# Optimization experiments

Measured on AMD Instinct MI355X. Metric: run time of the kernel, lower is better.

Reference implementation:

```python
import jax, jax.numpy as jnp
import numpy as np

B, T, C = 2, 2048, 768
N_HEADS = 12
HEAD = C // N_HEADS


def setup_inputs() -> dict:
    key = jax.random.key(0)
    k1, k2, k3 = jax.random.split(key, 3)
    x = jax.random.normal(k1, (B, T, C), dtype=jnp.float32)
    # torch Linear weights: [out_features, in_features]
    W_attn = jax.random.normal(k2, (3 * C, C), dtype=jnp.float32) * 0.02
    W_proj = jax.random.normal(k3, (C, C), dtype=jnp.float32) * 0.02
    return {"x": x, "W_attn": W_attn, "W_proj": W_proj}


def reference(x, W_attn, W_proj):
    b, t, c = x.shape
    qkv = jnp.einsum('btc,oc->bto', x, W_attn)  # [B,T,3C]
    q, k, v = jnp.split(qkv, 3, axis=-1)
    # [B, H, T, D]
    q = q.reshape(b, t, N_HEADS, HEAD).transpose(0, 2, 1, 3)
    k = k.reshape(b, t, N_HEADS, HEAD).transpose(0, 2, 1, 3)
    v = v.reshape(b, t, N_HEADS, HEAD).transpose(0, 2, 1, 3)
    scale = 1.0 / jnp.sqrt(jnp.asarray(HEAD, dtype=x.dtype))
    wei = jnp.einsum('bhqd,bhkd->bhqk', q, k) * scale  # [B,H,T,T]
    causal = jnp.tril(jnp.ones((t, t), dtype=bool))
    wei = jnp.where(causal[None, None], wei, jnp.asarray(-jnp.inf, dtype=wei.dtype))
    wei = jax.nn.softmax(wei, axis=-1)  # dropout p=0 -> identity
    out = jnp.einsum('bhqk,bhkd->bhqd', wei, v)
    out = out.transpose(0, 2, 1, 3).reshape(b, t, c)
    out = jnp.einsum('btc,oc->bto', out, W_proj)
    return out
```

## Files before the change

kernel.cpp:

```cpp
#include <hip/hip_runtime.h>

#define T_DIM 2048
#define C_DIM 768
#define NH    12
#define HD    64
#define KDIM  768
#define JOBS_PER_XCD 96

typedef __attribute__((ext_vector_type(8))) short short8;
typedef __attribute__((ext_vector_type(4))) float f32x4;
typedef unsigned short u16;

__device__ __forceinline__ u16 f2bf(float f) {
    unsigned int u = __builtin_bit_cast(unsigned int, f);
    u = (u + 0x7fffu + ((u >> 16) & 1u)) >> 16;
    return (u16)u;
}
__device__ __forceinline__ f32x4 max4(f32x4 a, f32x4 b) {
    f32x4 r; r[0]=fmaxf(a[0],b[0]); r[1]=fmaxf(a[1],b[1]);
    r[2]=fmaxf(a[2],b[2]); r[3]=fmaxf(a[3],b[3]); return r;
}
__device__ __forceinline__ unsigned int cvtpk(float a, float b) {
    unsigned int r;
    asm("v_cvt_pk_bf16_f32 %0, %1, %2" : "=v"(r) : "v"(a), "v"(b));
    return r;
}
__device__ __forceinline__ void gload16(const u16* g, u16* l) {
    __builtin_amdgcn_global_load_lds(
        (const __attribute__((address_space(1))) unsigned int*)g,
        (__attribute__((address_space(3))) unsigned int*)l, 16, 0, 0);
}

#define NX  (4096 * 768)
#define NWA (2304 * 768)
#define NWP (768 * 768)
#define TOT4 ((NX + NWA + NWP) / 4)

__global__ __launch_bounds__(256) void convert_all(
    const float* __restrict__ x, const float* __restrict__ wa,
    const float* __restrict__ wp, u16* __restrict__ xb,
    u16* __restrict__ wab, u16* __restrict__ wpb, int* __restrict__ counters)
{
    if (blockIdx.x == 0 && threadIdx.x < 8) counters[threadIdx.x] = 0;
    for (int i4 = blockIdx.x * 256 + threadIdx.x; i4 < TOT4; i4 += gridDim.x * 256) {
        int i = i4 * 4;
        const float* src; u16* dst; int off;
        if (i < NX)            { src = x;  dst = xb;  off = i; }
        else if (i < NX + NWA) { src = wa; dst = wab; off = i - NX; }
        else                   { src = wp; dst = wpb; off = i - NX - NWA; }
        float4 v = *(const float4*)&src[off];
        ushort4 o;
        o.x = f2bf(v.x); o.y = f2bf(v.y); o.z = f2bf(v.z); o.w = f2bf(v.w);
        *(ushort4*)&dst[off] = o;
    }
}

__global__ __launch_bounds__(256) void gemm_qkv(
    const u16* __restrict__ A, const u16* __restrict__ Wt,
    u16* __restrict__ qb, u16* __restrict__ kb, u16* __restrict__ vtb)
{
    __shared__ __align__(16) u16 AsL[2][128][32];
    __shared__ __align__(16) u16 BsL[2][128][32];

    const int tid = threadIdx.x;
    const int orig = blockIdx.x;
    const int wg = (orig & 7) * 72 + (orig >> 3);
    const int bm = (wg / 18) * 128;
    const int bn = (wg % 18) * 128;

    const int w = tid >> 6, l = tid & 63;
    const int wr = (w >> 1) * 64, wc = (w & 1) * 64;
    const int lrow = l & 15, lg = l >> 4;
    const int lr4 = l >> 2, lc4 = l & 3;

    f32x4 acc[4][4];
    const f32x4 zero4 = {0.f, 0.f, 0.f, 0.f};
#pragma unroll
    for (int mi = 0; mi < 4; ++mi)
#pragma unroll
        for (int ni = 0; ni < 4; ++ni) acc[mi][ni] = zero4;

    auto STAGE = [&](int buf, int k0) {
#pragma unroll
        for (int i = 0; i < 2; ++i) {
            const int rb = w * 32 + i * 16;
            const int row = rb + lr4;
            const int sc = (lc4 ^ (row & 3)) * 8;
            gload16(&A [(size_t)(bm + row) * KDIM + k0 + sc], &AsL[buf][rb][0]);
            gload16(&Wt[(size_t)(bn + row) * KDIM + k0 + sc], &BsL[buf][rb][0]);
        }
    };

    int cur = 0;
    STAGE(0, 0);
    for (int k0 = 0; k0 < KDIM; k0 += 32) {
        __syncthreads();
        if (k0 + 32 < KDIM) STAGE(cur ^ 1, k0 + 32);

        short8 af[4], bf[4];
#pragma unroll
        for (int mi = 0; mi < 4; ++mi)
            af[mi] = *(const short8*)&AsL[cur][wr + mi * 16 + lrow][(lg ^ (lrow & 3)) * 8];
#pragma unroll
        for (int ni = 0; ni < 4; ++ni)
            bf[ni] = *(const short8*)&BsL[cur][wc + ni * 16 + lrow][(lg ^ (lrow & 3)) * 8];
#pragma unroll
        for (int mi = 0; mi < 4; ++mi)
#pragma unroll
            for (int ni = 0; ni < 4; ++ni)
                acc[mi][ni] = __builtin_amdgcn_mfma_f32_16x16x32_bf16(
                    af[mi], bf[ni], acc[mi][ni], 0, 0, 0);
        cur ^= 1;
    }

#pragma unroll
    for (int ni = 0; ni < 4; ++ni) {
        const int colbase = bn + wc + ni * 16;
        const int which = colbase / C_DIM;
        const int h = (colbase % C_DIM) / HD;
        const int d = (colbase % HD) + lrow;
        const float qs = (which == 0) ? 0.18033688011112042f : 1.0f;
#pragma unroll
        for (int mi = 0; mi < 4; ++mi) {
            const int t0 = bm + wr + mi * 16 + lg * 4;
            const int bb2 = t0 >> 11, tt = t0 & 2047;
            const size_t bhoff = (size_t)(bb2 * NH + h);
            if (which == 2) {
                ushort4 pv;
                pv.x = f2bf(acc[mi][ni][0]); pv.y = f2bf(acc[mi][ni][1]);
                pv.z = f2bf(acc[mi][ni][2]); pv.w = f2bf(acc[mi][ni][3]);
                *(ushort4*)&vtb[(bhoff * HD + d) * T_DIM + tt] = pv;
            } else {
                u16* dst = (which == 0) ? qb : kb;
#pragma unroll
                for (int jj = 0; jj < 4; ++jj)
                    dst[(bhoff * T_DIM + tt + jj) * HD + d] = f2bf(acc[mi][ni][jj] * qs);
            }
        }
    }
}

__global__ __launch_bounds__(256) void gemm_proj(
    const u16* __restrict__ A, const u16* __restrict__ Wt,
    float* __restrict__ dense)
{
    __shared__ __align__(16) u16 As[64][40];
    __shared__ __align__(16) u16 Bs[128][40];

    const int tid = threadIdx.x;
    const int orig = blockIdx.x;
    const int wg = (orig & 7) * 48 + (orig >> 3);
    const int bm = (wg / 6) * 64, bn = (wg % 6) * 128;

    const int w = tid >> 6, l = tid & 63;
    const int wr = (w >> 1) * 32, wc = (w & 1) * 64;
    const int lrow = l & 15, lg = l >> 4;

    const int srow = tid >> 2;
    const int scol = (tid & 3) * 8;

    f32x4 acc[2][4];
    const f32x4 zero4 = {0.f, 0.f, 0.f, 0.f};
#pragma unroll
    for (int mi = 0; mi < 2; ++mi)
#pragma unroll
        for (int ni = 0; ni < 4; ++ni) acc[mi][ni] = zero4;

    uint4 ra0 = *(const uint4*)&A [(size_t)(bm + srow)      * KDIM + scol];
    uint4 rb0 = *(const uint4*)&Wt[(size_t)(bn + srow)      * KDIM + scol];
    uint4 rb1 = *(const uint4*)&Wt[(size_t)(bn + 64 + srow) * KDIM + scol];

    for (int k0 = 0; k0 < KDIM; k0 += 32) {
        __syncthreads();
        *(uint4*)&As[srow][scol]      = ra0;
        *(uint4*)&Bs[srow][scol]      = rb0;
        *(uint4*)&Bs[64 + srow][scol] = rb1;
        __syncthreads();

        if (k0 + 32 < KDIM) {
            ra0 = *(const uint4*)&A [(size_t)(bm + srow)      * KDIM + k0 + 32 + scol];
            rb0 = *(const uint4*)&Wt[(size_t)(bn + srow)      * KDIM + k0 + 32 + scol];
            rb1 = *(const uint4*)&Wt[(size_t)(bn + 64 + srow) * KDIM + k0 + 32 + scol];
        }

        short8 af[2], bf[4];
#pragma unroll
        for (int mi = 0; mi < 2; ++mi)
            af[mi] = *(const short8*)&As[wr + mi * 16 + lrow][lg * 8];
#pragma unroll
        for (int ni = 0; ni < 4; ++ni)
            bf[ni] = *(const short8*)&Bs[wc + ni * 16 + lrow][lg * 8];
#pragma unroll
        for (int mi = 0; mi < 2; ++mi)
#pragma unroll
            for (int ni = 0; ni < 4; ++ni)
                acc[mi][ni] = __builtin_amdgcn_mfma_f32_16x16x32_bf16(
                    af[mi], bf[ni], acc[mi][ni], 0, 0, 0);
    }

#pragma unroll
    for (int ni = 0; ni < 4; ++ni) {
        const int col = bn + wc + ni * 16 + lrow;
#pragma unroll
        for (int mi = 0; mi < 2; ++mi) {
            const int m0 = bm + wr + mi * 16 + lg * 4;
#pragma unroll
            for (int jj = 0; jj < 4; ++jj)
                dense[(size_t)(m0 + jj) * C_DIM + col] = acc[mi][ni][jj];
        }
    }
}

__global__ __launch_bounds__(256, 2) void attn_mfma(
    const u16* __restrict__ q, const u16* __restrict__ k,
    const u16* __restrict__ vt, u16* __restrict__ aw, int* __restrict__ counters)
{
    __shared__ __align__(16) u16 KsL [2][128][64];
    __shared__ __align__(16) u16 VtsL[2][64][128];
    __shared__ __align__(16) u16 Ps  [4][16][72];
    __shared__ int job_s;

    const int tid = threadIdx.x, w = tid >> 6, l = tid & 63;
    const int lrow = l & 15, lg = l >> 4;
    const int lr8 = l >> 3, lc8 = l & 7;
    const int lr16 = l >> 4, lc16 = l & 15;
    const int xcdi = blockIdx.x & 7;
    const f32x4 zero4 = {0.f, 0.f, 0.f, 0.f};

    for (;;) {
        __syncthreads();
        if (tid == 0) job_s = atomicAdd(&counters[xcdi], 1);
        __syncthreads();
        const int j = job_s;
        if (j >= JOBS_PER_XCD) break;

        const int qt = 31 - (j / 3);
        const int bh = xcdi * 3 + (j - (j / 3) * 3);
        const int bb = bh / NH, hh = bh % NH;
        const int qbase = qt * 64 + w * 16;
        const int qg = qbase + lrow;

        const u16* Qp = q  + (size_t)bh * T_DIM * HD;
        const u16* Kp = k  + (size_t)bh * T_DIM * HD;
        const u16* Vp = vt + (size_t)bh * HD * T_DIM;

        const short8 aq0 = *(const short8*)&Qp[(size_t)(qbase + lrow) * HD + lg * 8];
        const short8 aq1 = *(const short8*)&Qp[(size_t)(qbase + lrow) * HD + 32 + lg * 8];

        f32x4 o0[4], o1[4];
#pragma unroll
        for (int n = 0; n < 4; ++n) { o0[n] = zero4; o1[n] = zero4; }
        float m0 = -3.0e38f, l0 = 0.0f;
        float m1 = -3.0e38f, l1 = 0.0f;

        auto STAGE = [&](int buf, int kk0) {
#pragma unroll
            for (int i = 0; i < 4; ++i) {
                const int rb = w * 32 + i * 8;
                const int row = rb + lr8;
                gload16(&Kp[(size_t)(kk0 + row) * HD + ((lc8 ^ (row & 7)) * 8)],
                        &KsL[buf][rb][0]);
            }
#pragma unroll
            for (int i = 0; i < 4; ++i) {
                const int db = w * 16 + i * 4;
                const int d = db + lr16;
                gload16(&Vp[(size_t)d * T_DIM + kk0 + ((lc16 ^ (d & 15)) * 8)],
                        &VtsL[buf][db][0]);
            }
        };

        auto PROCESS = [&](f32x4* s, int sub, int kk0, bool masked,
                           float& mr, float& lr_, f32x4* oo) {
            if (masked) {
#pragma unroll
                for (int n = 0; n < 4; ++n)
#pragma unroll
                    for (int jj = 0; jj < 4; ++jj)
                        if (kk0 + sub * 64 + n * 16 + lg * 4 + jj > qg)
                            s[n][jj] = -3.0e38f;
            }
            f32x4 t2 = max4(max4(s[0], s[1]), max4(s[2], s[3]));
            float rm = fmaxf(fmaxf(t2[0], t2[1]), fmaxf(t2[2], t2[3]));
            rm = fmaxf(rm, __shfl_xor(rm, 16));
            rm = fmaxf(rm, __shfl_xor(rm, 32));
            const float m_new = fmaxf(mr, rm);
            const float alpha = exp2f(mr - m_new);
            mr = m_new;
#pragma unroll
            for (int n = 0; n < 4; ++n)
#pragma unroll
                for (int jj = 0; jj < 4; ++jj)
                    s[n][jj] = exp2f(s[n][jj] - m_new);
            f32x4 a2 = (s[0] + s[1]) + (s[2] + s[3]);
            float rs = (a2[0] + a2[1]) + (a2[2] + a2[3]);
            rs += __shfl_xor(rs, 16);
            rs += __shfl_xor(rs, 32);
            lr_ = lr_ * alpha + rs;
#pragma unroll
            for (int n = 0; n < 4; ++n) {
                uint2 pr;
                pr.x = cvtpk(s[n][0], s[n][1]);
                pr.y = cvtpk(s[n][2], s[n][3]);
                *(uint2*)&Ps[w][lrow][n * 16 + lg * 4] = pr;
            }
#pragma unroll
            for (int jj = 0; jj < 4; ++jj) {
                const float aj = __shfl(alpha, lg * 4 + jj);
                oo[0][jj] *= aj; oo[1][jj] *= aj; oo[2][jj] *= aj; oo[3][jj] *= aj;
            }
            const short8 ap0 = *(const short8*)&Ps[w][lrow][lg * 8];
            const short8 ap1 = *(const short8*)&Ps[w][lrow][32 + lg * 8];
            const int cur = (kk0 >> 7) & 1;
#pragma unroll
            for (int n = 0; n < 4; ++n) {
                const int row = n * 16 + lrow;
                const short8 bv0 = *(const short8*)
                    &VtsL[cur][row][((sub * 8 + lg) ^ lrow) * 8];
                const short8 bv1 = *(const short8*)
                    &VtsL[cur][row][((sub * 8 + 4 + lg) ^ lrow) * 8];
                oo[n] = __builtin_amdgcn_mfma_f32_16x16x32_bf16(ap0, bv0, oo[n], 0, 0, 0);
                oo[n] = __builtin_amdgcn_mfma_f32_16x16x32_bf16(ap1, bv1, oo[n], 0, 0, 0);
            }
        };

        const int nkt = qt / 2 + 1;
        int cur = 0;
        STAGE(0, 0);
        for (int kt = 0; kt < nkt; ++kt) {
            const int kk0 = kt * 128;
            __syncthreads();
            if (kt + 1 < nkt) STAGE(cur ^ 1, kk0 + 128);

            const bool last = (kt == nkt - 1);
            const int nsub = (last && (qt & 1) == 0) ? 1 : 2;

            f32x4 s0[4], s1[4];
#pragma unroll
            for (int n = 0; n < 4; ++n) {
                const int row = n * 16 + lrow;
                const short8 kf0 = *(const short8*)&KsL[cur][row][((lg)     ^ (lrow & 7)) * 8];
                const short8 kf1 = *(const short8*)&KsL[cur][row][((lg + 4) ^ (lrow & 7)) * 8];
                s0[n] = __builtin_amdgcn_mfma_f32_16x16x32_bf16(kf0, aq0, zero4, 0, 0, 0);
                s0[n] = __builtin_amdgcn_mfma_f32_16x16x32_bf16(kf1, aq1, s0[n], 0, 0, 0);
            }
            if (nsub == 2) {
#pragma unroll
                for (int n = 0; n < 4; ++n) {
                    const int row = 64 + n * 16 + lrow;
                    const short8 kf0 = *(const short8*)&KsL[cur][row][((lg)     ^ (lrow & 7)) * 8];
                    const short8 kf1 = *(const short8*)&KsL[cur][row][((lg + 4) ^ (lrow & 7)) * 8];
                    s1[n] = __builtin_amdgcn_mfma_f32_16x16x32_bf16(kf0, aq0, zero4, 0, 0, 0);
                    s1[n] = __builtin_amdgcn_mfma_f32_16x16x32_bf16(kf1, aq1, s1[n], 0, 0, 0);
                }
            }

            PROCESS(s0, 0, kk0, last && nsub == 1, m0, l0, o0);
            if (nsub == 2) PROCESS(s1, 1, kk0, last, m1, l1, o1);

            cur ^= 1;
        }

        const float mf = fmaxf(m0, m1);
        const float a0 = exp2f(m0 - mf);
        const float a1 = exp2f(m1 - mf);
        const float inv = 1.0f / (l0 * a0 + l1 * a1);
#pragma unroll
        for (int jj = 0; jj < 4; ++jj) {
            const int qrow = lg * 4 + jj;
            const float a0j = __shfl(a0, qrow);
            const float a1j = __shfl(a1, qrow);
            const float invj = __shfl(inv, qrow);
            const size_t m = (size_t)bb * T_DIM + qbase + qrow;
#pragma unroll
            for (int n = 0; n < 4; ++n)
                aw[m * C_DIM + hh * HD + n * 16 + lrow] =
                    f2bf((o0[n][jj] * a0j + o1[n][jj] * a1j) * invj);
        }
    }
}

extern "C" void kernel_launch(void* const* d_in, const int* in_sizes, int n_in,
                              void* d_out, int out_size, void* d_ws, size_t ws_size,
                              hipStream_t stream) {
    const float* x      = (const float*)d_in[0];
    const float* W_attn = (const float*)d_in[1];
    const float* W_proj = (const float*)d_in[2];
    float* out = (float*)d_out;

    char* ws = (char*)d_ws;
    u16* xb  = (u16*)ws;                       ws += (size_t)NX * 2;
    u16* wab = (u16*)ws;                       ws += (size_t)NWA * 2;
    u16* wpb = (u16*)ws;                       ws += (size_t)NWP * 2;
    u16* qb  = (u16*)ws;                       ws += (size_t)24 * T_DIM * HD * 2;
    u16* kb  = (u16*)ws;                       ws += (size_t)24 * T_DIM * HD * 2;
    u16* vtb = (u16*)ws;                       ws += (size_t)24 * T_DIM * HD * 2;
    u16* awb = (u16*)ws;                       ws += (size_t)4096 * C_DIM * 2;
    int* cnt = (int*)ws;

    convert_all<<<2048, 256, 0, stream>>>(x, W_attn, W_proj, xb, wab, wpb, cnt);

    gemm_qkv<<<576, 256, 0, stream>>>(xb, wab, qb, kb, vtb);

    attn_mfma<<<512, 256, 0, stream>>>(qb, kb, vtb, awb, cnt);

    gemm_proj<<<384, 256, 0, stream>>>(awb, wpb, out);
}
```

Baseline: 99.17 us.

## Schedule attention per wave with direct global K/V fragment loads instead of LDS

The attention kernel now has each wave claim its own job: 32 query rows for one batch-head, split into two 16-row groups. Jobs come from a per-XCD atomic counter padded onto separate cache lines, replacing the block-wide atomic and its two barriers. K and V fragments are read straight from global memory into registers and shared by both query groups, so LDS double buffering and per-tile __syncthreads are gone. This removes block-level synchronisation and gives finer-grained load balance across the causal triangle, at the cost of losing the asynchronous prefetch and cross-wave K/V reuse through LDS, which leaves more load latency exposed.

```diff
diff --git a/kernel.cpp b/kernel.cpp
--- a/kernel.cpp
+++ b/kernel.cpp
@@ -5,7 +5,7 @@
 #define NH    12
 #define HD    64
 #define KDIM  768
-#define JOBS_PER_XCD 96
+#define JOBS_PER_XCD 192
 
 typedef __attribute__((ext_vector_type(8))) short short8;
 typedef __attribute__((ext_vector_type(4))) float f32x4;
@@ -41,7 +41,7 @@
     const float* __restrict__ wp, u16* __restrict__ xb,
     u16* __restrict__ wab, u16* __restrict__ wpb, int* __restrict__ counters)
 {
-    if (blockIdx.x == 0 && threadIdx.x < 8) counters[threadIdx.x] = 0;
+    if (blockIdx.x == 0 && threadIdx.x < 8) counters[threadIdx.x * 16] = 0;
     for (int i4 = blockIdx.x * 256 + threadIdx.x; i4 < TOT4; i4 += gridDim.x * 256) {
         int i = i4 * 4;
         const float* src; u16* dst; int off;
@@ -215,70 +215,48 @@
     const u16* __restrict__ q, const u16* __restrict__ k,
     const u16* __restrict__ vt, u16* __restrict__ aw, int* __restrict__ counters)
 {
-    __shared__ __align__(16) u16 KsL [2][128][64];
-    __shared__ __align__(16) u16 VtsL[2][64][128];
-    __shared__ __align__(16) u16 Ps  [4][16][72];
-    __shared__ int job_s;
+    __shared__ __align__(16) u16 Ps[4][16][72];
 
     const int tid = threadIdx.x, w = tid >> 6, l = tid & 63;
     const int lrow = l & 15, lg = l >> 4;
-    const int lr8 = l >> 3, lc8 = l & 7;
-    const int lr16 = l >> 4, lc16 = l & 15;
     const int xcdi = blockIdx.x & 7;
     const f32x4 zero4 = {0.f, 0.f, 0.f, 0.f};
 
     for (;;) {
-        __syncthreads();
-        if (tid == 0) job_s = atomicAdd(&counters[xcdi], 1);
-        __syncthreads();
-        const int j = job_s;
+        int j0 = 0;
+        if (l == 0) j0 = atomicAdd(&counters[xcdi * 16], 1);
+        const int j = __shfl(j0, 0);
         if (j >= JOBS_PER_XCD) break;
 
-        const int qt = 31 - (j / 3);
+        const int rt = 63 - j / 3;
         const int bh = xcdi * 3 + (j - (j / 3) * 3);
         const int bb = bh / NH, hh = bh % NH;
-        const int qbase = qt * 64 + w * 16;
-        const int qg = qbase + lrow;
+        const int q0 = rt * 32;
 
         const u16* Qp = q  + (size_t)bh * T_DIM * HD;
         const u16* Kp = k  + (size_t)bh * T_DIM * HD;
         const u16* Vp = vt + (size_t)bh * HD * T_DIM;
 
-        const short8 aq0 = *(const short8*)&Qp[(size_t)(qbase + lrow) * HD + lg * 8];
-        const short8 aq1 = *(const short8*)&Qp[(size_t)(qbase + lrow) * HD + 32 + lg * 8];
-
-        f32x4 o0[4], o1[4];
-#pragma unroll
-        for (int n = 0; n < 4; ++n) { o0[n] = zero4; o1[n] = zero4; }
-        float m0 = -3.0e38f, l0 = 0.0f;
-        float m1 = -3.0e38f, l1 = 0.0f;
-
-        auto STAGE = [&](int buf, int kk0) {
-#pragma unroll
-            for (int i = 0; i < 4; ++i) {
-                const int rb = w * 32 + i * 8;
-                const int row = rb + lr8;
-                gload16(&Kp[(size_t)(kk0 + row) * HD + ((lc8 ^ (row & 7)) * 8)],
-                        &KsL[buf][rb][0]);
-            }
-#pragma unroll
-            for (int i = 0; i < 4; ++i) {
-                const int db = w * 16 + i * 4;
-                const int d = db + lr16;
-                gload16(&Vp[(size_t)d * T_DIM + kk0 + ((lc16 ^ (d & 15)) * 8)],
-                        &VtsL[buf][db][0]);
-            }
-        };
-
-        auto PROCESS = [&](f32x4* s, int sub, int kk0, bool masked,
-                           float& mr, float& lr_, f32x4* oo) {
+        const short8 aqA0 = *(const short8*)&Qp[(size_t)(q0 + lrow) * HD + lg * 8];
+        const short8 aqA1 = *(const short8*)&Qp[(size_t)(q0 + lrow) * HD + 32 + lg * 8];
+        const short8 aqB0 = *(const short8*)&Qp[(size_t)(q0 + 16 + lrow) * HD + lg * 8];
+        const short8 aqB1 = *(const short8*)&Qp[(size_t)(q0 + 16 + lrow) * HD + 32 + lg * 8];
+
+        f32x4 oA[4], oB[4];
+#pragma unroll
+        for (int n = 0; n < 4; ++n) { oA[n] = zero4; oB[n] = zero4; }
+        float mA = -3.0e38f, lA = 0.0f;
+        float mB = -3.0e38f, lB = 0.0f;
+
+        auto PROC = [&](f32x4* s, int goff, bool masked, int kb,
+                        float& mr, float& lr_, f32x4* oo, const short8* vf) {
             if (masked) {
+                const int qg = q0 + goff + lrow;
 #pragma unroll
                 for (int n = 0; n < 4; ++n)
 #pragma unroll
                     for (int jj = 0; jj < 4; ++jj)
-                        if (kk0 + sub * 64 + n * 16 + lg * 4 + jj > qg)
-                            s[n][jj] = -3.0e38f;
+                        if (kb + n * 16 + lg * 4 + jj > qg) s[n][jj] = -3.0e38f;
             }
             f32x4 t2 = max4(max4(s[0], s[1]), max4(s[2], s[3]));
             float rm = fmaxf(fmaxf(t2[0], t2[1]), fmaxf(t2[2], t2[3]));
@@ -311,71 +289,62 @@
             }
             const short8 ap0 = *(const short8*)&Ps[w][lrow][lg * 8];
             const short8 ap1 = *(const short8*)&Ps[w][lrow][32 + lg * 8];
-            const int cur = (kk0 >> 7) & 1;
-#pragma unroll
-            for (int n = 0; n < 4; ++n) {
-                const int row = n * 16 + lrow;
-                const short8 bv0 = *(const short8*)
-                    &VtsL[cur][row][((sub * 8 + lg) ^ lrow) * 8];
-                const short8 bv1 = *(const short8*)
-                    &VtsL[cur][row][((sub * 8 + 4 + lg) ^ lrow) * 8];
-                oo[n] = __builtin_amdgcn_mfma_f32_16x16x32_bf16(ap0, bv0, oo[n], 0, 0, 0);
-                oo[n] = __builtin_amdgcn_mfma_f32_16x16x32_bf16(ap1, bv1, oo[n], 0, 0, 0);
+#pragma unroll
+            for (int n = 0; n < 4; ++n) {
+                oo[n] = __builtin_amdgcn_mfma_f32_16x16x32_bf16(ap0, vf[2 * n],     oo[n], 0, 0, 0);
+                oo[n] = __builtin_amdgcn_mfma_f32_16x16x32_bf16(ap1, vf[2 * n + 1], oo[n], 0, 0, 0);
             }
         };
 
-        const int nkt = qt / 2 + 1;
-        int cur = 0;
-        STAGE(0, 0);
-        for (int kt = 0; kt < nkt; ++kt) {
-            const int kk0 = kt * 128;
-            __syncthreads();
-            if (kt + 1 < nkt) STAGE(cur ^ 1, kk0 + 128);
-
-            const bool last = (kt == nkt - 1);
-            const int nsub = (last && (qt & 1) == 0) ? 1 : 2;
-
-            f32x4 s0[4], s1[4];
-#pragma unroll
-            for (int n = 0; n < 4; ++n) {
-                const int row = n * 16 + lrow;
-                const short8 kf0 = *(const short8*)&KsL[cur][row][((lg)     ^ (lrow & 7)) * 8];
-                const short8 kf1 = *(const short8*)&KsL[cur][row][((lg + 4) ^ (lrow & 7)) * 8];
-                s0[n] = __builtin_amdgcn_mfma_f32_16x16x32_bf16(kf0, aq0, zero4, 0, 0, 0);
-                s0[n] = __builtin_amdgcn_mfma_f32_16x16x32_bf16(kf1, aq1, s0[n], 0, 0, 0);
-            }
-            if (nsub == 2) {
-#pragma unroll
-                for (int n = 0; n < 4; ++n) {
-                    const int row = 64 + n * 16 + lrow;
-                    const short8 kf0 = *(const short8*)&KsL[cur][row][((lg)     ^ (lrow & 7)) * 8];
-                    const short8 kf1 = *(const short8*)&KsL[cur][row][((lg + 4) ^ (lrow & 7)) * 8];
-                    s1[n] = __builtin_amdgcn_mfma_f32_16x16x32_bf16(kf0, aq0, zero4, 0, 0, 0);
-                    s1[n] = __builtin_amdgcn_mfma_f32_16x16x32_bf16(kf1, aq1, s1[n], 0, 0, 0);
-                }
-            }
-
-            PROCESS(s0, 0, kk0, last && nsub == 1, m0, l0, o0);
-            if (nsub == 2) PROCESS(s1, 1, kk0, last, m1, l1, o1);
-
-            cur ^= 1;
-        }
-
-        const float mf = fmaxf(m0, m1);
-        const float a0 = exp2f(m0 - mf);
-        const float a1 = exp2f(m1 - mf);
-        const float inv = 1.0f / (l0 * a0 + l1 * a1);
+        const int nsb = (q0 + 95) / 64;
+        for (int sb = 0; sb < nsb; ++sb) {
+            const int kb = sb * 64;
+            const bool masked = (sb == nsb - 1);
+
+            short8 kf[8];
+#pragma unroll
+            for (int n = 0; n < 4; ++n) {
+                kf[2 * n]     = *(const short8*)&Kp[(size_t)(kb + n * 16 + lrow) * HD + lg * 8];
+                kf[2 * n + 1] = *(const short8*)&Kp[(size_t)(kb + n * 16 + lrow) * HD + 32 + lg * 8];
+            }
+
+            f32x4 sA[4], sB[4];
+#pragma unroll
+            for (int n = 0; n < 4; ++n) {
+                sA[n] = __builtin_amdgcn_mfma_f32_16x16x32_bf16(kf[2 * n],     aqA0, zero4, 0, 0, 0);
+                sA[n] = __builtin_amdgcn_mfma_f32_16x16x32_bf16(kf[2 * n + 1], aqA1, sA[n], 0, 0, 0);
+            }
+#pragma unroll
+            for (int n = 0; n < 4; ++n) {
+                sB[n] = __builtin_amdgcn_mfma_f32_16x16x32_bf16(kf[2 * n],     aqB0, zero4, 0, 0, 0);
+                sB[n] = __builtin_amdgcn_mfma_f32_16x16x32_bf16(kf[2 * n + 1], aqB1, sB[n], 0, 0, 0);
+            }
+
+            short8 vf[8];
+#pragma unroll
+            for (int n = 0; n < 4; ++n) {
+                vf[2 * n]     = *(const short8*)&Vp[(size_t)(n * 16 + lrow) * T_DIM + kb + lg * 8];
+                vf[2 * n + 1] = *(const short8*)&Vp[(size_t)(n * 16 + lrow) * T_DIM + kb + 32 + lg * 8];
+            }
+
+            PROC(sA, 0,  masked, kb, mA, lA, oA, vf);
+            PROC(sB, 16, masked, kb, mB, lB, oB, vf);
+        }
+
 #pragma unroll
         for (int jj = 0; jj < 4; ++jj) {
             const int qrow = lg * 4 + jj;
-            const float a0j = __shfl(a0, qrow);
-            const float a1j = __shfl(a1, qrow);
-            const float invj = __shfl(inv, qrow);
-            const size_t m = (size_t)bb * T_DIM + qbase + qrow;
-#pragma unroll
-            for (int n = 0; n < 4; ++n)
-                aw[m * C_DIM + hh * HD + n * 16 + lrow] =
-                    f2bf((o0[n][jj] * a0j + o1[n][jj] * a1j) * invj);
+            const float lAj = __shfl(lA, qrow);
+            const float lBj = __shfl(lB, qrow);
+            const float invA = 1.0f / lAj;
+            const float invB = 1.0f / lBj;
+            const size_t mAi = (size_t)bb * T_DIM + q0 + qrow;
+            const size_t mBi = (size_t)bb * T_DIM + q0 + 16 + qrow;
+#pragma unroll
+            for (int n = 0; n < 4; ++n) {
+                aw[mAi * C_DIM + hh * HD + n * 16 + lrow] = f2bf(oA[n][jj] * invA);
+                aw[mBi * C_DIM + hh * HD + n * 16 + lrow] = f2bf(oB[n][jj] * invB);
+            }
         }
     }
 }
```

After: 146.0 us. 47.2% more time.
